# Kernel optimization log

Hardware: AMD Instinct MI355X
Metric: run time of the kernel (lower is better)

Reference implementation:

```python
import jax, jax.numpy as jnp
import numpy as np

N = 1024          # num nodes
IN_DIM = 1024     # model dim
H = 16            # num heads
HD = IN_DIM // H  # head dim = 64
L = 4             # max_path_len
D_EDGE = 64       # edge feature dim
E = 16384         # num edges
NUM_ET = 8        # num edge types
SCALE = 1.0 / np.sqrt(HD)


def setup_inputs() -> dict:
    key = jax.random.key(0)
    ks = jax.random.split(key, 16)
    s = 0.02
    return {
        "node_feat": jax.random.normal(ks[0], (N, IN_DIM), jnp.float32),
        "edge_feat": jax.random.normal(ks[1], (E, D_EDGE), jnp.float32),
        "distances": jax.random.uniform(ks[2], (N, N), jnp.float32),
        "shortest_distances": jax.random.randint(ks[3], (N, N), 0, L + 2),
        "shortest_paths": jax.random.randint(ks[4], (N, N, L), 0, E + 1),
        "edge_type": jax.random.randint(ks[5], (N, N), 0, NUM_ET),
        "Wq": jax.random.normal(ks[6], (IN_DIM, IN_DIM), jnp.float32) * s,
        "bq": jnp.zeros((IN_DIM,), jnp.float32),
        "Wk": jax.random.normal(ks[7], (IN_DIM, IN_DIM), jnp.float32) * s,
        "bk": jnp.zeros((IN_DIM,), jnp.float32),
        "Wv": jax.random.normal(ks[8], (IN_DIM, IN_DIM), jnp.float32) * s,
        "bv": jnp.zeros((IN_DIM,), jnp.float32),
        "Wo": jax.random.normal(ks[9], (IN_DIM, IN_DIM), jnp.float32) * s,
        "bo": jnp.zeros((IN_DIM,), jnp.float32),
        "spatial_table": jax.random.normal(ks[10], (L + 1, H), jnp.float32) * s,  # SpatialEncoding bias emb reshaped
        "edge_weight": jax.random.normal(ks[11], (L, H, D_EDGE), jnp.float32) * s,  # EdgeEncoding weight emb
    }


def reference(node_feat, edge_feat, distances, shortest_distances, shortest_paths,
              edge_type, Wq, bq, Wk, bk, Wv, bv, Wo, bo, spatial_table, edge_weight):
    # projections (torch Linear stored as [in,out] here)
    Q = (node_feat @ Wq + bq).reshape(N, H, HD)
    K = (node_feat @ Wk + bk).reshape(N, H, HD)
    V = (node_feat @ Wv + bv).reshape(N, H, HD)

    # QK^T / sqrt(d), laid out [N_q, N_k, H] as in the original permute(1,2,0)
    score = jnp.einsum('nhd,mhd->nmh', Q, K) * SCALE

    # spatial encoding: per-pair bias gathered by clamped shortest distance
    score = score + spatial_table[jnp.clip(shortest_distances, 0, L)]  # [N,N,H]

    # edge encoding: gather per-path edge features from padded table, contract with
    # per-(path-position, head) weight vectors. Pre-contract per edge to avoid the
    # [N,N,L,D] intermediate: C[e,l,h] = padded_edge_feat[e] . edge_weight[l,h].
    pad_ef = jnp.concatenate([edge_feat, jnp.zeros((1, D_EDGE), edge_feat.dtype)], axis=0)
    C = jnp.einsum('ed,lhd->elh', pad_ef, edge_weight)                 # [E+1, L, H]
    l_idx = jnp.arange(L)
    edge_enc = C[shortest_paths, l_idx[None, None, :]].sum(axis=2)     # gather [N,N,L,H] -> sum -> [N,N,H]
    score = score + edge_enc

    # mask unreachable / self pairs (shortest_distances <= 0)
    mask = shortest_distances <= 0
    score = jnp.where(mask[:, :, None], -jnp.inf, score)

    # softmax over key axis (intended attention normalization; see notes)
    attn = jax.nn.softmax(score, axis=1)                               # [N_q, N_k, H]

    out = jnp.einsum('nmh,mhd->nhd', attn, V).reshape(N, IN_DIM)
    return out @ Wo + bo
```

## Files before the change

kernel.cpp:

```cpp
#include <hip/hip_runtime.h>
#include <math.h>

#define N_    1024
#define H_    16
#define E_    16384
#define SCALE 0.125f

typedef unsigned short u16;
typedef unsigned int   u32;
typedef short  short8v __attribute__((ext_vector_type(8)));
typedef float  f32x4   __attribute__((ext_vector_type(4)));
typedef u16    u16x4   __attribute__((ext_vector_type(4)));
typedef u16    u16x8   __attribute__((ext_vector_type(8)));

__device__ __forceinline__ u16 f2bf(float f) {
    union { float f; unsigned u; } v; v.f = f;
    unsigned r = v.u + 0x7fffu + ((v.u >> 16) & 1u);
    return (u16)(r >> 16);
}
__device__ __forceinline__ float bf2f(u16 u) {
    union { unsigned u; float f; } v; v.u = (u32)u << 16; return v.f;
}

template<int U64>
__device__ __forceinline__ void stage_bt(const u16* __restrict__ g, int ldr,
                                         u16* s, int tid)
{
    const int l = tid & 63, w = tid >> 6;
    for (int c = w; c < U64; c += 4) {
        int o16 = (c << 6) + l;
        int row = o16 >> 3;
        int ss  = (o16 & 7) ^ (row & 7);
        const u16* gp = g + (size_t)row * ldr + (ss << 3);
        u16* lp = s + (c << 9);
        __builtin_amdgcn_global_load_lds(
            (const __attribute__((address_space(1))) void*)gp,
            (__attribute__((address_space(3))) void*)lp, 16, 0, 0);
    }
}

__device__ __forceinline__ short8v frag_read(const u16* s, int row, int slot) {
    return *(const short8v*)(s + row * 64 + ((slot ^ (row & 7)) << 3));
}

template<int NT>
__device__ __forceinline__ void gemm_bt_core(
    const u16* __restrict__ At, int lda,
    const u16* __restrict__ Bt, int ldb,
    int K, u16* As, u16* Bs, f32x4 (&acc)[4][NT/32], int tid)
{
    const int l  = tid & 63;
    const int wm = tid >> 7, wn = (tid >> 6) & 1;
    const int lr = l & 15,   lk = l >> 4;
    for (int k0 = 0; k0 < K; k0 += 64) {
        if (k0) __syncthreads();
        stage_bt<16>(At + k0, lda, As, tid);
        stage_bt<NT/8>(Bt + k0, ldb, Bs, tid);
        __syncthreads();
        #pragma unroll
        for (int s = 0; s < 2; ++s) {
            short8v af[4], bfv[NT/32];
            #pragma unroll
            for (int i = 0; i < 4; ++i)
                af[i] = frag_read(As, wm*64 + i*16 + lr, s*4 + lk);
            #pragma unroll
            for (int j = 0; j < NT/32; ++j)
                bfv[j] = frag_read(Bs, wn*(NT/2) + j*16 + lr, s*4 + lk);
            #pragma unroll
            for (int i = 0; i < 4; ++i)
                #pragma unroll
                for (int j = 0; j < NT/32; ++j)
                    asm("v_mfma_f32_16x16x32_bf16 %0, %1, %2, %0"
                        : "+v"(acc[i][j]) : "v"(af[i]), "v"(bfv[j]));
        }
    }
    __syncthreads();
}

__global__ __launch_bounds__(256) void conv_x(const float* __restrict__ X,
                                              u16* __restrict__ Xb)
{
    size_t i = (size_t)blockIdx.x * 256 + threadIdx.x;
    float4 a = ((const float4*)X)[2*i], b = ((const float4*)X)[2*i + 1];
    u16x8 o;
    o[0]=f2bf(a.x); o[1]=f2bf(a.y); o[2]=f2bf(a.z); o[3]=f2bf(a.w);
    o[4]=f2bf(b.x); o[5]=f2bf(b.y); o[6]=f2bf(b.z); o[7]=f2bf(b.w);
    *(u16x8*)&Xb[8*i] = o;
}

__global__ __launch_bounds__(256) void conv_wt(
    const float* __restrict__ Wq, const float* __restrict__ Wk,
    const float* __restrict__ Wv, const float* __restrict__ Wo,
    u16* __restrict__ Wt)
{
    __shared__ u16 tile[64][65];
    const int t = threadIdx.x;
    const int n0 = blockIdx.x*64, k0 = blockIdx.y*64, mz = blockIdx.z;
    const float* W = mz==0 ? Wq : mz==1 ? Wk : mz==2 ? Wv : Wo;
    u16* Wd = Wt + (size_t)mz * 1024 * 1024;
    #pragma unroll
    for (int p = 0; p < 4; ++p) {
        int r = p*16 + (t>>4), c = (t&15)*4;
        float4 v = *(const float4*)&W[(size_t)(k0+r)*1024 + n0 + c];
        tile[c+0][r]=f2bf(v.x); tile[c+1][r]=f2bf(v.y);
        tile[c+2][r]=f2bf(v.z); tile[c+3][r]=f2bf(v.w);
    }
    __syncthreads();
    #pragma unroll
    for (int p = 0; p < 4; ++p) {
        int nr = p*16 + (t>>4), kc = (t&15)*4;
        u16x4 o = { tile[nr][kc], tile[nr][kc+1], tile[nr][kc+2], tile[nr][kc+3] };
        *(u16x4*)&Wd[(size_t)(n0+nr)*1024 + k0 + kc] = o;
    }
}

__global__ __launch_bounds__(256) void transpose_v(const u16* __restrict__ Vb,
                                                   u16* __restrict__ Vt)
{
    __shared__ u16 tile[64][65];
    const int t = threadIdx.x;
    const int c0 = blockIdx.x*64, r0 = blockIdx.y*64;
    #pragma unroll
    for (int p = 0; p < 4; ++p) {
        int r = p*16 + (t>>4), c = (t&15)*4;
        u16x4 v = *(const u16x4*)&Vb[(size_t)(r0+r)*1024 + c0 + c];
        tile[c+0][r]=v[0]; tile[c+1][r]=v[1]; tile[c+2][r]=v[2]; tile[c+3][r]=v[3];
    }
    __syncthreads();
    #pragma unroll
    for (int p = 0; p < 4; ++p) {
        int cr = p*16 + (t>>4), rc = (t&15)*4;
        u16x4 o = { tile[cr][rc], tile[cr][rc+1], tile[cr][rc+2], tile[cr][rc+3] };
        *(u16x4*)&Vt[(size_t)(c0+cr)*1024 + r0 + rc] = o;
    }
}

__global__ __launch_bounds__(256) void edge_pre_kernel(
    const float* __restrict__ EF, const float* __restrict__ EW, u16* __restrict__ C)
{
    __shared__ float ews[64][66];
    __shared__ float ef[16][64];
    const int t = threadIdx.x;
    const int e0 = blockIdx.x * 16;
    #pragma unroll
    for (int i = 0; i < 16; ++i) {
        int idx = t + i * 256;
        ews[idx >> 6][idx & 63] = EW[idx];
    }
    #pragma unroll
    for (int i = 0; i < 4; ++i) {
        int idx = t + i * 256;
        int r = idx >> 6, d = idx & 63;
        int e = e0 + r;
        ef[r][d] = (e < E_) ? EF[(size_t)e * 64 + d] : 0.f;
    }
    __syncthreads();
    const int lh = t & 63;
    const int rb = t >> 6;
    #pragma unroll
    for (int j = 0; j < 4; ++j) {
        int r = rb * 4 + j;
        int e = e0 + r;
        if (e > E_) continue;
        float acc = 0.f;
        if (e < E_) {
            #pragma unroll
            for (int d = 0; d < 64; ++d) acc += ef[r][d] * ews[lh][d];
        }
        C[(size_t)e * 64 + lh] = f2bf(acc);
    }
}

__global__ __launch_bounds__(256) void qkv_gemm(
    const u16* __restrict__ Xb, const u16* __restrict__ Wt,
    const float* __restrict__ bq, const float* __restrict__ bk,
    const float* __restrict__ bv,
    u16* __restrict__ Qb, u16* __restrict__ Kb, u16* __restrict__ Vb)
{
    __shared__ u16 As[128*64], Bs[128*64];
    const int tid = threadIdx.x;
    const int col0 = blockIdx.x * 128, row0 = blockIdx.y * 128;
    f32x4 acc[4][4] = {};
    gemm_bt_core<128>(Xb + (size_t)row0*1024, 1024,
                      Wt + (size_t)col0*1024, 1024, 1024, As, Bs, acc, tid);
    const int l = tid & 63, wm = tid>>7, wn = (tid>>6)&1, lr = l&15, lk = l>>4;
    const int sel = col0 >> 10;
    const float* bias = sel==0 ? bq : sel==1 ? bk : bv;
    u16* O = sel==0 ? Qb : sel==1 ? Kb : Vb;
    const int cbase = col0 & 1023;
    #pragma unroll
    for (int j = 0; j < 4; ++j) {
        int cc = cbase + wn*64 + j*16 + lr;
        float bb = bias[cc];
        #pragma unroll
        for (int i = 0; i < 4; ++i) {
            int rg = row0 + wm*64 + i*16 + lk*4;
            #pragma unroll
            for (int r = 0; r < 4; ++r)
                O[(size_t)(rg + r)*1024 + cc] = f2bf(acc[i][j][r] + bb);
        }
    }
}

__global__ __launch_bounds__(256) void qk_gemm(
    const u16* __restrict__ Qb, const u16* __restrict__ Kb, float* __restrict__ S)
{
    __shared__ u16 As[128*64], Bs[128*64];
    const int tid = threadIdx.x;
    const int col0 = blockIdx.x*128, row0 = blockIdx.y*128, h = blockIdx.z;
    f32x4 acc[4][4] = {};
    gemm_bt_core<128>(Qb + (size_t)row0*1024 + h*64, 1024,
                      Kb + (size_t)col0*1024 + h*64, 1024, 64, As, Bs, acc, tid);
    const int l = tid & 63, wm = tid>>7, wn = (tid>>6)&1, lr = l&15, lk = l>>4;
    float* So = S + ((size_t)h << 20);
    #pragma unroll
    for (int j = 0; j < 4; ++j) {
        int cg = col0 + wn*64 + j*16 + lr;
        #pragma unroll
        for (int i = 0; i < 4; ++i) {
            int rg = row0 + wm*64 + i*16 + lk*4;
            #pragma unroll
            for (int r = 0; r < 4; ++r)
                So[(size_t)(rg + r)*1024 + cg] = acc[i][j][r] * SCALE;
        }
    }
}

__global__ __launch_bounds__(256) void pv_gemm(
    const u16* __restrict__ P, const u16* __restrict__ Vt, u16* __restrict__ AO)
{
    __shared__ u16 As[128*64], Bs[64*64];
    const int tid = threadIdx.x;
    const int row0 = blockIdx.x * 128, h = blockIdx.y;
    f32x4 acc[4][2] = {};
    gemm_bt_core<64>(P + ((size_t)((h<<10) + row0)) * 2048, 2048,
                     Vt + (size_t)h*64*1024, 1024, 1024, As, Bs, acc, tid);
    const int l = tid & 63, wm = tid>>7, wn = (tid>>6)&1, lr = l&15, lk = l>>4;
    #pragma unroll
    for (int j = 0; j < 2; ++j) {
        int col = h*64 + wn*32 + j*16 + lr;
        #pragma unroll
        for (int i = 0; i < 4; ++i) {
            int rg = row0 + wm*64 + i*16 + lk*4;
            #pragma unroll
            for (int r = 0; r < 4; ++r)
                AO[(size_t)(rg + r)*1024 + col] = f2bf(acc[i][j][r]);
        }
    }
}

__global__ __launch_bounds__(256) void out_gemm(
    const u16* __restrict__ AO, const u16* __restrict__ Wot,
    const float* __restrict__ bo, float* __restrict__ out)
{
    __shared__ u16 As[128*64], Bs[128*64];
    const int tid = threadIdx.x;
    const int col0 = blockIdx.x * 128, row0 = blockIdx.y * 128;
    f32x4 acc[4][4] = {};
    gemm_bt_core<128>(AO + (size_t)row0*1024, 1024,
                      Wot + (size_t)col0*1024, 1024, 1024, As, Bs, acc, tid);
    const int l = tid & 63, wm = tid>>7, wn = (tid>>6)&1, lr = l&15, lk = l>>4;
    #pragma unroll
    for (int j = 0; j < 4; ++j) {
        int cg = col0 + wn*64 + j*16 + lr;
        float bb = bo[cg];
        #pragma unroll
        for (int i = 0; i < 4; ++i) {
            int rg = row0 + wm*64 + i*16 + lk*4;
            #pragma unroll
            for (int r = 0; r < 4; ++r)
                out[(size_t)(rg + r)*1024 + cg] = acc[i][j][r] + bb;
        }
    }
}

__global__ __launch_bounds__(512) void bias_softmax7(
    const int* __restrict__ SD, const int* __restrict__ SP,
    const u16* __restrict__ C, const float* __restrict__ STBL,
    float* __restrict__ S)
{
    __shared__ int   sdl[1024];
    __shared__ float stbl[80];
    __shared__ float bias[8][1024];
    const int t = threadIdx.x;
    const int n = blockIdx.x;
    const int w = t >> 6, lane = t & 63;
    #pragma unroll
    for (int k = 0; k < 2; ++k) {
        int m = t + k*512;
        sdl[m] = SD[(size_t)n*1024 + m];
    }
    const int4 v0 = *(const int4*)&SP[((size_t)n*1024 + t)*4];
    const int4 v1 = *(const int4*)&SP[((size_t)n*1024 + t + 512)*4];
    if (t < 80) stbl[t] = STBL[t];

    float2 pre0[8], pre1[8];
    {
        const float* sr0 = S + (((size_t)w << 10) + n) * 1024;
        const float* sr1 = S + (((size_t)(w + 8) << 10) + n) * 1024;
        #pragma unroll
        for (int j = 0; j < 8; ++j) pre0[j] = *(const float2*)&sr0[lane*2 + j*128];
        #pragma unroll
        for (int j = 0; j < 8; ++j) pre1[j] = *(const float2*)&sr1[lane*2 + j*128];
    }
    __syncthreads();

    #pragma unroll
    for (int hc = 0; hc < 16; hc += 8) {
        if (hc) __syncthreads();
        #pragma unroll
        for (int k = 0; k < 2; ++k) {
            int m   = t + k*512;
            int4 e4 = k ? v1 : v0;
            int sdv = sdl[m];
            int cl  = sdv > 4 ? 4 : (sdv < 0 ? 0 : sdv);
            float4 b0 = *(const float4*)&stbl[cl*16 + hc];
            float4 b1 = *(const float4*)&stbl[cl*16 + hc + 4];
            u16x8 A0 = *(const u16x8*)&C[(size_t)e4.x*64 +  0 + hc];
            u16x8 D0 = *(const u16x8*)&C[(size_t)e4.y*64 + 16 + hc];
            u16x8 F0 = *(const u16x8*)&C[(size_t)e4.z*64 + 32 + hc];
            u16x8 G0 = *(const u16x8*)&C[(size_t)e4.w*64 + 48 + hc];
            bias[0][m] = b0.x + bf2f(A0[0]) + bf2f(D0[0]) + bf2f(F0[0]) + bf2f(G0[0]);
            bias[1][m] = b0.y + bf2f(A0[1]) + bf2f(D0[1]) + bf2f(F0[1]) + bf2f(G0[1]);
            bias[2][m] = b0.z + bf2f(A0[2]) + bf2f(D0[2]) + bf2f(F0[2]) + bf2f(G0[2]);
            bias[3][m] = b0.w + bf2f(A0[3]) + bf2f(D0[3]) + bf2f(F0[3]) + bf2f(G0[3]);
            bias[4][m] = b1.x + bf2f(A0[4]) + bf2f(D0[4]) + bf2f(F0[4]) + bf2f(G0[4]);
            bias[5][m] = b1.y + bf2f(A0[5]) + bf2f(D0[5]) + bf2f(F0[5]) + bf2f(G0[5]);
            bias[6][m] = b1.z + bf2f(A0[6]) + bf2f(D0[6]) + bf2f(F0[6]) + bf2f(G0[6]);
            bias[7][m] = b1.w + bf2f(A0[7]) + bf2f(D0[7]) + bf2f(F0[7]) + bf2f(G0[7]);
        }
        __syncthreads();
        const int h = hc + w;
        float* srow = S + (((size_t)h << 10) + n) * 1024;
        float v[16];
        float lmax = -INFINITY;
        #pragma unroll
        for (int j = 0; j < 8; ++j) {
            int m = lane*2 + j*128;
            float2 sv = hc ? pre1[j] : pre0[j];
            float2 bb = *(const float2*)&bias[w][m];
            int2 sd2 = *(const int2*)&sdl[m];
            float x0 = (sd2.x <= 0) ? -INFINITY : sv.x + bb.x;
            float x1 = (sd2.y <= 0) ? -INFINITY : sv.y + bb.y;
            v[2*j] = x0; v[2*j+1] = x1;
            lmax = fmaxf(lmax, fmaxf(x0, x1));
        }
        #pragma unroll
        for (int o = 32; o; o >>= 1) lmax = fmaxf(lmax, __shfl_xor(lmax, o));
        float lsum = 0.f;
        #pragma unroll
        for (int j = 0; j < 16; ++j) { v[j] = __expf(v[j] - lmax); lsum += v[j]; }
        #pragma unroll
        for (int o = 32; o; o >>= 1) lsum += __shfl_xor(lsum, o);
        float inv = 1.f / lsum;
        u16* prow = (u16*)srow;
        #pragma unroll
        for (int j = 0; j < 8; ++j) {
            int m = lane*2 + j*128;
            u32 pk = ((u32)f2bf(v[2*j+1] * inv) << 16) | f2bf(v[2*j] * inv);
            *(u32*)&prow[m] = pk;
        }
    }
}

extern "C" void kernel_launch(void* const* d_in, const int* in_sizes, int n_in,
                              void* d_out, int out_size, void* d_ws, size_t ws_size,
                              hipStream_t stream)
{
    const float* node_feat = (const float*)d_in[0];
    const float* edge_feat = (const float*)d_in[1];
    const int*   sd        = (const int*)d_in[3];
    const int*   sp        = (const int*)d_in[4];
    const float* Wq = (const float*)d_in[6];
    const float* bq = (const float*)d_in[7];
    const float* Wk = (const float*)d_in[8];
    const float* bk = (const float*)d_in[9];
    const float* Wv = (const float*)d_in[10];
    const float* bv = (const float*)d_in[11];
    const float* Wo = (const float*)d_in[12];
    const float* bo = (const float*)d_in[13];
    const float* spatial = (const float*)d_in[14];
    const float* ew      = (const float*)d_in[15];
    float* out = (float*)d_out;

    char* base = (char*)d_ws;
    u16*   Xb = (u16*)(base);
    u16*   Qb = (u16*)(base + ((size_t)2 << 20));
    u16*   Kb = (u16*)(base + ((size_t)4 << 20));
    u16*   Vb = (u16*)(base + ((size_t)6 << 20));
    u16*   Wt = (u16*)(base + ((size_t)8 << 20));
    u16*   C  = (u16*)(base + ((size_t)16 << 20));
    float* S  = (float*)(base + ((size_t)19 << 20));
    u16*   Vt = Xb;
    u16*   AO = Qb;

    conv_x<<<512, 256, 0, stream>>>(node_feat, Xb);
    conv_wt<<<dim3(16,16,4), 256, 0, stream>>>(Wq, Wk, Wv, Wo, Wt);
    edge_pre_kernel<<<dim3(E_/16 + 1), 256, 0, stream>>>(edge_feat, ew, C);
    qkv_gemm<<<dim3(24,8), 256, 0, stream>>>(Xb, Wt, bq, bk, bv, Qb, Kb, Vb);
    transpose_v<<<dim3(16,16), 256, 0, stream>>>(Vb, Vt);
    qk_gemm<<<dim3(8,8,16), 256, 0, stream>>>(Qb, Kb, S);
    bias_softmax7<<<dim3(1024), 512, 0, stream>>>(sd, sp, C, spatial, S);
    pv_gemm<<<dim3(8,16), 256, 0, stream>>>((const u16*)S, Vt, AO);
    out_gemm<<<dim3(8,8), 256, 0, stream>>>(AO, Wt + (size_t)3*1024*1024, bo, out);
}
```

Before: 147.6 us.

## Shrink GEMM tiles for more blocks and prefetch edge-bias gathers early

```diff
diff --git a/kernel.cpp b/kernel.cpp
--- a/kernel.cpp
+++ b/kernel.cpp
@@ -43,31 +43,31 @@
     return *(const short8v*)(s + row * 64 + ((slot ^ (row & 7)) << 3));
 }
 
-template<int NT>
+template<int MT, int NT>
 __device__ __forceinline__ void gemm_bt_core(
     const u16* __restrict__ At, int lda,
     const u16* __restrict__ Bt, int ldb,
-    int K, u16* As, u16* Bs, f32x4 (&acc)[4][NT/32], int tid)
+    int K, u16* As, u16* Bs, f32x4 (&acc)[MT/32][NT/32], int tid)
 {
     const int l  = tid & 63;
     const int wm = tid >> 7, wn = (tid >> 6) & 1;
     const int lr = l & 15,   lk = l >> 4;
     for (int k0 = 0; k0 < K; k0 += 64) {
         if (k0) __syncthreads();
-        stage_bt<16>(At + k0, lda, As, tid);
+        stage_bt<MT/8>(At + k0, lda, As, tid);
         stage_bt<NT/8>(Bt + k0, ldb, Bs, tid);
         __syncthreads();
         #pragma unroll
         for (int s = 0; s < 2; ++s) {
-            short8v af[4], bfv[NT/32];
-            #pragma unroll
-            for (int i = 0; i < 4; ++i)
-                af[i] = frag_read(As, wm*64 + i*16 + lr, s*4 + lk);
+            short8v af[MT/32], bfv[NT/32];
+            #pragma unroll
+            for (int i = 0; i < MT/32; ++i)
+                af[i] = frag_read(As, wm*(MT/2) + i*16 + lr, s*4 + lk);
             #pragma unroll
             for (int j = 0; j < NT/32; ++j)
                 bfv[j] = frag_read(Bs, wn*(NT/2) + j*16 + lr, s*4 + lk);
             #pragma unroll
-            for (int i = 0; i < 4; ++i)
+            for (int i = 0; i < MT/32; ++i)
                 #pragma unroll
                 for (int j = 0; j < NT/32; ++j)
                     asm("v_mfma_f32_16x16x32_bf16 %0, %1, %2, %0"
@@ -177,12 +177,12 @@
     const float* __restrict__ bv,
     u16* __restrict__ Qb, u16* __restrict__ Kb, u16* __restrict__ Vb)
 {
-    __shared__ u16 As[128*64], Bs[128*64];
+    __shared__ u16 As[64*64], Bs[128*64];
     const int tid = threadIdx.x;
-    const int col0 = blockIdx.x * 128, row0 = blockIdx.y * 128;
-    f32x4 acc[4][4] = {};
-    gemm_bt_core<128>(Xb + (size_t)row0*1024, 1024,
-                      Wt + (size_t)col0*1024, 1024, 1024, As, Bs, acc, tid);
+    const int col0 = blockIdx.x * 128, row0 = blockIdx.y * 64;
+    f32x4 acc[2][4] = {};
+    gemm_bt_core<64,128>(Xb + (size_t)row0*1024, 1024,
+                         Wt + (size_t)col0*1024, 1024, 1024, As, Bs, acc, tid);
     const int l = tid & 63, wm = tid>>7, wn = (tid>>6)&1, lr = l&15, lk = l>>4;
     const int sel = col0 >> 10;
     const float* bias = sel==0 ? bq : sel==1 ? bk : bv;
@@ -193,8 +193,8 @@
         int cc = cbase + wn*64 + j*16 + lr;
         float bb = bias[cc];
         #pragma unroll
-        for (int i = 0; i < 4; ++i) {
-            int rg = row0 + wm*64 + i*16 + lk*4;
+        for (int i = 0; i < 2; ++i) {
+            int rg = row0 + wm*32 + i*16 + lk*4;
             #pragma unroll
             for (int r = 0; r < 4; ++r)
                 O[(size_t)(rg + r)*1024 + cc] = f2bf(acc[i][j][r] + bb);
@@ -209,8 +209,8 @@
     const int tid = threadIdx.x;
     const int col0 = blockIdx.x*128, row0 = blockIdx.y*128, h = blockIdx.z;
     f32x4 acc[4][4] = {};
-    gemm_bt_core<128>(Qb + (size_t)row0*1024 + h*64, 1024,
-                      Kb + (size_t)col0*1024 + h*64, 1024, 64, As, Bs, acc, tid);
+    gemm_bt_core<128,128>(Qb + (size_t)row0*1024 + h*64, 1024,
+                          Kb + (size_t)col0*1024 + h*64, 1024, 64, As, Bs, acc, tid);
     const int l = tid & 63, wm = tid>>7, wn = (tid>>6)&1, lr = l&15, lk = l>>4;
     float* So = S + ((size_t)h << 20);
     #pragma unroll
@@ -229,19 +229,19 @@
 __global__ __launch_bounds__(256) void pv_gemm(
     const u16* __restrict__ P, const u16* __restrict__ Vt, u16* __restrict__ AO)
 {
-    __shared__ u16 As[128*64], Bs[64*64];
+    __shared__ u16 As[64*64], Bs[64*64];
     const int tid = threadIdx.x;
-    const int row0 = blockIdx.x * 128, h = blockIdx.y;
-    f32x4 acc[4][2] = {};
-    gemm_bt_core<64>(P + ((size_t)((h<<10) + row0)) * 2048, 2048,
-                     Vt + (size_t)h*64*1024, 1024, 1024, As, Bs, acc, tid);
+    const int row0 = blockIdx.x * 64, h = blockIdx.y;
+    f32x4 acc[2][2] = {};
+    gemm_bt_core<64,64>(P + ((size_t)((h<<10) + row0)) * 2048, 2048,
+                        Vt + (size_t)h*64*1024, 1024, 1024, As, Bs, acc, tid);
     const int l = tid & 63, wm = tid>>7, wn = (tid>>6)&1, lr = l&15, lk = l>>4;
     #pragma unroll
     for (int j = 0; j < 2; ++j) {
         int col = h*64 + wn*32 + j*16 + lr;
         #pragma unroll
-        for (int i = 0; i < 4; ++i) {
-            int rg = row0 + wm*64 + i*16 + lk*4;
+        for (int i = 0; i < 2; ++i) {
+            int rg = row0 + wm*32 + i*16 + lk*4;
             #pragma unroll
             for (int r = 0; r < 4; ++r)
                 AO[(size_t)(rg + r)*1024 + col] = f2bf(acc[i][j][r]);
@@ -253,20 +253,20 @@
     const u16* __restrict__ AO, const u16* __restrict__ Wot,
     const float* __restrict__ bo, float* __restrict__ out)
 {
-    __shared__ u16 As[128*64], Bs[128*64];
+    __shared__ u16 As[64*64], Bs[64*64];
     const int tid = threadIdx.x;
-    const int col0 = blockIdx.x * 128, row0 = blockIdx.y * 128;
-    f32x4 acc[4][4] = {};
-    gemm_bt_core<128>(AO + (size_t)row0*1024, 1024,
-                      Wot + (size_t)col0*1024, 1024, 1024, As, Bs, acc, tid);
+    const int col0 = blockIdx.x * 64, row0 = blockIdx.y * 64;
+    f32x4 acc[2][2] = {};
+    gemm_bt_core<64,64>(AO + (size_t)row0*1024, 1024,
+                        Wot + (size_t)col0*1024, 1024, 1024, As, Bs, acc, tid);
     const int l = tid & 63, wm = tid>>7, wn = (tid>>6)&1, lr = l&15, lk = l>>4;
     #pragma unroll
-    for (int j = 0; j < 4; ++j) {
-        int cg = col0 + wn*64 + j*16 + lr;
+    for (int j = 0; j < 2; ++j) {
+        int cg = col0 + wn*32 + j*16 + lr;
         float bb = bo[cg];
         #pragma unroll
-        for (int i = 0; i < 4; ++i) {
-            int rg = row0 + wm*64 + i*16 + lk*4;
+        for (int i = 0; i < 2; ++i) {
+            int rg = row0 + wm*32 + i*16 + lk*4;
             #pragma unroll
             for (int r = 0; r < 4; ++r)
                 out[(size_t)(rg + r)*1024 + cg] = acc[i][j][r] + bb;
@@ -274,7 +274,7 @@
     }
 }
 
-__global__ __launch_bounds__(512) void bias_softmax7(
+__global__ __launch_bounds__(512) void bias_softmax8(
     const int* __restrict__ SD, const int* __restrict__ SP,
     const u16* __restrict__ C, const float* __restrict__ STBL,
     float* __restrict__ S)
@@ -303,33 +303,60 @@
         #pragma unroll
         for (int j = 0; j < 8; ++j) pre1[j] = *(const float2*)&sr1[lane*2 + j*128];
     }
-    __syncthreads();
-
+    u16x8 g1[2][4], g2[2][4];
+    #pragma unroll
+    for (int k = 0; k < 2; ++k) {
+        int4 e4 = k ? v1 : v0;
+        g1[k][0] = *(const u16x8*)&C[(size_t)e4.x*64 +  0];
+        g1[k][1] = *(const u16x8*)&C[(size_t)e4.y*64 + 16];
+        g1[k][2] = *(const u16x8*)&C[(size_t)e4.z*64 + 32];
+        g1[k][3] = *(const u16x8*)&C[(size_t)e4.w*64 + 48];
+        g2[k][0] = *(const u16x8*)&C[(size_t)e4.x*64 +  0 + 8];
+        g2[k][1] = *(const u16x8*)&C[(size_t)e4.y*64 + 16 + 8];
+        g2[k][2] = *(const u16x8*)&C[(size_t)e4.z*64 + 32 + 8];
+        g2[k][3] = *(const u16x8*)&C[(size_t)e4.w*64 + 48 + 8];
+    }
+    __syncthreads();
+
+    #pragma unroll
+    for (int k = 0; k < 2; ++k) {
+        int m   = t + k*512;
+        int sdv = sdl[m];
+        int cl  = sdv > 4 ? 4 : (sdv < 0 ? 0 : sdv);
+        float4 b0 = *(const float4*)&stbl[cl*16];
+        float4 b1 = *(const float4*)&stbl[cl*16 + 4];
+        bias[0][m] = b0.x + bf2f(g1[k][0][0]) + bf2f(g1[k][1][0]) + bf2f(g1[k][2][0]) + bf2f(g1[k][3][0]);
+        bias[1][m] = b0.y + bf2f(g1[k][0][1]) + bf2f(g1[k][1][1]) + bf2f(g1[k][2][1]) + bf2f(g1[k][3][1]);
+        bias[2][m] = b0.z + bf2f(g1[k][0][2]) + bf2f(g1[k][1][2]) + bf2f(g1[k][2][2]) + bf2f(g1[k][3][2]);
+        bias[3][m] = b0.w + bf2f(g1[k][0][3]) + bf2f(g1[k][1][3]) + bf2f(g1[k][2][3]) + bf2f(g1[k][3][3]);
+        bias[4][m] = b1.x + bf2f(g1[k][0][4]) + bf2f(g1[k][1][4]) + bf2f(g1[k][2][4]) + bf2f(g1[k][3][4]);
+        bias[5][m] = b1.y + bf2f(g1[k][0][5]) + bf2f(g1[k][1][5]) + bf2f(g1[k][2][5]) + bf2f(g1[k][3][5]);
+        bias[6][m] = b1.z + bf2f(g1[k][0][6]) + bf2f(g1[k][1][6]) + bf2f(g1[k][2][6]) + bf2f(g1[k][3][6]);
+        bias[7][m] = b1.w + bf2f(g1[k][0][7]) + bf2f(g1[k][1][7]) + bf2f(g1[k][2][7]) + bf2f(g1[k][3][7]);
+    }
+    __syncthreads();
     #pragma unroll
     for (int hc = 0; hc < 16; hc += 8) {
-        if (hc) __syncthreads();
-        #pragma unroll
-        for (int k = 0; k < 2; ++k) {
-            int m   = t + k*512;
-            int4 e4 = k ? v1 : v0;
-            int sdv = sdl[m];
-            int cl  = sdv > 4 ? 4 : (sdv < 0 ? 0 : sdv);
-            float4 b0 = *(const float4*)&stbl[cl*16 + hc];
-            float4 b1 = *(const float4*)&stbl[cl*16 + hc + 4];
-            u16x8 A0 = *(const u16x8*)&C[(size_t)e4.x*64 +  0 + hc];
-            u16x8 D0 = *(const u16x8*)&C[(size_t)e4.y*64 + 16 + hc];
-            u16x8 F0 = *(const u16x8*)&C[(size_t)e4.z*64 + 32 + hc];
-            u16x8 G0 = *(const u16x8*)&C[(size_t)e4.w*64 + 48 + hc];
-            bias[0][m] = b0.x + bf2f(A0[0]) + bf2f(D0[0]) + bf2f(F0[0]) + bf2f(G0[0]);
-            bias[1][m] = b0.y + bf2f(A0[1]) + bf2f(D0[1]) + bf2f(F0[1]) + bf2f(G0[1]);
-            bias[2][m] = b0.z + bf2f(A0[2]) + bf2f(D0[2]) + bf2f(F0[2]) + bf2f(G0[2]);
-            bias[3][m] = b0.w + bf2f(A0[3]) + bf2f(D0[3]) + bf2f(F0[3]) + bf2f(G0[3]);
-            bias[4][m] = b1.x + bf2f(A0[4]) + bf2f(D0[4]) + bf2f(F0[4]) + bf2f(G0[4]);
-            bias[5][m] = b1.y + bf2f(A0[5]) + bf2f(D0[5]) + bf2f(F0[5]) + bf2f(G0[5]);
-            bias[6][m] = b1.z + bf2f(A0[6]) + bf2f(D0[6]) + bf2f(F0[6]) + bf2f(G0[6]);
-            bias[7][m] = b1.w + bf2f(A0[7]) + bf2f(D0[7]) + bf2f(F0[7]) + bf2f(G0[7]);
-        }
-        __syncthreads();
+        if (hc) {
+            __syncthreads();
+            #pragma unroll
+            for (int k = 0; k < 2; ++k) {
+                int m   = t + k*512;
+                int sdv = sdl[m];
+                int cl  = sdv > 4 ? 4 : (sdv < 0 ? 0 : sdv);
+                float4 b0 = *(const float4*)&stbl[cl*16 + 8];
+                float4 b1 = *(const float4*)&stbl[cl*16 + 12];
+                bias[0][m] = b0.x + bf2f(g2[k][0][0]) + bf2f(g2[k][1][0]) + bf2f(g2[k][2][0]) + bf2f(g2[k][3][0]);
+                bias[1][m] = b0.y + bf2f(g2[k][0][1]) + bf2f(g2[k][1][1]) + bf2f(g2[k][2][1]) + bf2f(g2[k][3][1]);
+                bias[2][m] = b0.z + bf2f(g2[k][0][2]) + bf2f(g2[k][1][2]) + bf2f(g2[k][2][2]) + bf2f(g2[k][3][2]);
+                bias[3][m] = b0.w + bf2f(g2[k][0][3]) + bf2f(g2[k][1][3]) + bf2f(g2[k][2][3]) + bf2f(g2[k][3][3]);
+                bias[4][m] = b1.x + bf2f(g2[k][0][4]) + bf2f(g2[k][1][4]) + bf2f(g2[k][2][4]) + bf2f(g2[k][3][4]);
+                bias[5][m] = b1.y + bf2f(g2[k][0][5]) + bf2f(g2[k][1][5]) + bf2f(g2[k][2][5]) + bf2f(g2[k][3][5]);
+                bias[6][m] = b1.z + bf2f(g2[k][0][6]) + bf2f(g2[k][1][6]) + bf2f(g2[k][2][6]) + bf2f(g2[k][3][6]);
+                bias[7][m] = b1.w + bf2f(g2[k][0][7]) + bf2f(g2[k][1][7]) + bf2f(g2[k][2][7]) + bf2f(g2[k][3][7]);
+            }
+            __syncthreads();
+        }
         const int h = hc + w;
         float* srow = S + (((size_t)h << 10) + n) * 1024;
         float v[16];
@@ -397,10 +424,10 @@
     conv_x<<<512, 256, 0, stream>>>(node_feat, Xb);
     conv_wt<<<dim3(16,16,4), 256, 0, stream>>>(Wq, Wk, Wv, Wo, Wt);
     edge_pre_kernel<<<dim3(E_/16 + 1), 256, 0, stream>>>(edge_feat, ew, C);
-    qkv_gemm<<<dim3(24,8), 256, 0, stream>>>(Xb, Wt, bq, bk, bv, Qb, Kb, Vb);
+    qkv_gemm<<<dim3(24,16), 256, 0, stream>>>(Xb, Wt, bq, bk, bv, Qb, Kb, Vb);
     transpose_v<<<dim3(16,16), 256, 0, stream>>>(Vb, Vt);
     qk_gemm<<<dim3(8,8,16), 256, 0, stream>>>(Qb, Kb, S);
-    bias_softmax7<<<dim3(1024), 512, 0, stream>>>(sd, sp, C, spatial, S);
-    pv_gemm<<<dim3(8,16), 256, 0, stream>>>((const u16*)S, Vt, AO);
-    out_gemm<<<dim3(8,8), 256, 0, stream>>>(AO, Wt + (size_t)3*1024*1024, bo, out);
-}
+    bias_softmax8<<<dim3(1024), 512, 0, stream>>>(sd, sp, C, spatial, S);
+    pv_gemm<<<dim3(16,16), 256, 0, stream>>>((const u16*)S, Vt, AO);
+    out_gemm<<<dim3(16,16), 256, 0, stream>>>(AO, Wt + (size_t)3*1024*1024, bo, out);
+}
```

New measurement: 127.7 us, median of 2. -13.5%, faster.
